# Optimization experiments

Hardware: AMD Instinct MI355X
Metric: run time of the kernel (lower is better)

The kernel has to match this reference:

```python
import jax, jax.numpy as jnp
import numpy as np

B, T, D, H = 2, 2048, 1024, 16
HD = D // H


def setup_inputs() -> dict:
    key = jax.random.key(0)
    ks = jax.random.split(key, 9)
    s = 1.0 / np.sqrt(D)
    return {
        "x": jax.random.normal(ks[0], (B, T, D), dtype=jnp.float32),
        "Wq": jax.random.normal(ks[1], (D, D), dtype=jnp.float32) * s,
        "bq": jnp.zeros((D,), dtype=jnp.float32),
        "Wk": jax.random.normal(ks[2], (D, D), dtype=jnp.float32) * s,
        "bk": jnp.zeros((D,), dtype=jnp.float32),
        "Wv": jax.random.normal(ks[3], (D, D), dtype=jnp.float32) * s,
        "bv": jnp.zeros((D,), dtype=jnp.float32),
        "Wo": jax.random.normal(ks[4], (D, D), dtype=jnp.float32) * s,
        "bo": jnp.zeros((D,), dtype=jnp.float32),
    }


def reference(x, Wq, bq, Wk, bk, Wv, bv, Wo, bo):
    b, t, d = x.shape
    # projections, split heads: (b, h, t, hd)
    def heads(y):
        return y.reshape(b, t, H, HD).transpose(0, 2, 1, 3)
    Q = heads(x @ Wq + bq)
    K = heads(x @ Wk + bk)
    V = heads(x @ Wv + bv)
    # scores scaled by sqrt(d) (full embed dim, faithful to source)
    score = jnp.einsum("bhid,bhjd->bhij", Q, K) / jnp.sqrt(jnp.float32(d))
    causal = jnp.triu(jnp.ones((t, t), dtype=bool), k=1)  # (t, t)
    score = jnp.where(causal, jnp.float32(-1e10), score)
    # FAITHFUL quirk: softmax over the HEAD axis (torch dim=1 of [b,h,t,t])
    weight = jax.nn.softmax(score, axis=1)
    out = jnp.einsum("bhij,bhjd->bhid", weight, V)
    out = out.transpose(0, 2, 1, 3).reshape(b, t, d)
    return out @ Wo + bo
```

## Files before the change

kernel.cpp:

```cpp
#include <hip/hip_runtime.h>
#include <hip/hip_bf16.h>

#define B_ 2
#define T_ 2048
#define D_ 1024
#define H_ 16

typedef __attribute__((ext_vector_type(8))) short bf16x8;
typedef __attribute__((ext_vector_type(4))) float f32x4;

__device__ __forceinline__ unsigned pack_bf16(float x, float y) {
  unsigned xb = __float_as_uint(x), yb = __float_as_uint(y);
  xb += 0x7fffu + ((xb >> 16) & 1u);
  yb += 0x7fffu + ((yb >> 16) & 1u);
  return (xb >> 16) | (yb & 0xffff0000u);
}
__device__ __forceinline__ unsigned short f2b(float x) {
  unsigned u = __float_as_uint(x);
  u += 0x7fffu + ((u >> 16) & 1u);
  return (unsigned short)(u >> 16);
}
__device__ __forceinline__ float blo(unsigned u) { return __uint_as_float(u << 16); }
__device__ __forceinline__ float bhi(unsigned u) { return __uint_as_float(u & 0xffff0000u); }

__device__ __forceinline__ void gld_lds16(const unsigned short* g, unsigned short* l) {
  __builtin_amdgcn_global_load_lds(
      (const __attribute__((address_space(1))) unsigned int*)g,
      (__attribute__((address_space(3))) unsigned int*)l, 16, 0, 0);
}

__global__ __launch_bounds__(256) void wtrans(const float* __restrict__ W0, const float* __restrict__ W1,
                                              const float* __restrict__ W2, const float* __restrict__ W3,
                                              unsigned short* __restrict__ T0, unsigned short* __restrict__ T1,
                                              unsigned short* __restrict__ T2, unsigned short* __restrict__ T3) {
  const int z = blockIdx.z;
  const float* W = z == 0 ? W0 : z == 1 ? W1 : z == 2 ? W2 : W3;
  unsigned short* T = z == 0 ? T0 : z == 1 ? T1 : z == 2 ? T2 : T3;
  __shared__ unsigned short t[64][72];
  const int k0 = blockIdx.x << 6, n0 = blockIdx.y << 6;
  const int r = threadIdx.x >> 2, c16 = (threadIdx.x & 3) << 4;
#pragma unroll
  for (int e = 0; e < 4; ++e) {
    const float4 v = *(const float4*)&W[(size_t)(k0 + r) * 1024 + n0 + c16 + e * 4];
    t[r][c16 + e * 4 + 0] = f2b(v.x);
    t[r][c16 + e * 4 + 1] = f2b(v.y);
    t[r][c16 + e * 4 + 2] = f2b(v.z);
    t[r][c16 + e * 4 + 3] = f2b(v.w);
  }
  __syncthreads();
  unsigned short o[16];
#pragma unroll
  for (int e = 0; e < 16; ++e) o[e] = t[c16 + e][r];
  unsigned short* dst = &T[(size_t)(n0 + r) * 1024 + k0 + c16];
  *(uint4*)&dst[0] = *(uint4*)&o[0];
  *(uint4*)&dst[8] = *(uint4*)&o[8];
}

__global__ __launch_bounds__(256) void xconv(const float* __restrict__ x, unsigned short* __restrict__ xb) {
  const int i = (blockIdx.x * 256 + threadIdx.x) * 8;
  const float4 a = *(const float4*)&x[i];
  const float4 b = *(const float4*)&x[i + 4];
  uint4 o;
  o.x = pack_bf16(a.x, a.y);
  o.y = pack_bf16(a.z, a.w);
  o.z = pack_bf16(b.x, b.y);
  o.w = pack_bf16(b.z, b.w);
  *(uint4*)&xb[i] = o;
}

template <bool BF16OUT>
__global__ __launch_bounds__(256) void gemm_mfma(const unsigned short* __restrict__ A,
                                                 const unsigned short* __restrict__ B0,
                                                 const unsigned short* __restrict__ B1,
                                                 const unsigned short* __restrict__ B2,
                                                 const float* __restrict__ bi0, const float* __restrict__ bi1,
                                                 const float* __restrict__ bi2,
                                                 void* __restrict__ Y0, void* __restrict__ Y1,
                                                 void* __restrict__ Y2) {
  const int z = blockIdx.z;
  const unsigned short* Bt = z == 0 ? B0 : z == 1 ? B1 : B2;
  const float* bias = z == 0 ? bi0 : z == 1 ? bi1 : bi2;
  void* Y = z == 0 ? Y0 : z == 1 ? Y1 : Y2;
  __shared__ unsigned short As[8192];
  __shared__ unsigned short Bs[8192];
  const int tid = threadIdx.x;
  const int m0 = blockIdx.y << 7, n0 = blockIdx.x << 7;
  const int w = tid >> 6, l = tid & 63, g = l >> 4, c = l & 15;
  const int wm = (w >> 1) << 6, wn = (w & 1) << 6;
  const int srow = tid >> 3;
  const int skel = ((tid & 7) ^ (srow & 7)) << 3;
  const unsigned short* ga = &A[(size_t)(m0 + srow) * 1024 + skel];
  const unsigned short* gb = &Bt[(size_t)(n0 + srow) * 1024 + skel];
  unsigned short* la = &As[tid << 3];
  unsigned short* lb = &Bs[tid << 3];
  f32x4 acc[4][4];
#pragma unroll
  for (int i = 0; i < 4; ++i)
#pragma unroll
    for (int j = 0; j < 4; ++j) acc[i][j] = {0.f, 0.f, 0.f, 0.f};
  for (int k0 = 0; k0 < 1024; k0 += 64) {
    __syncthreads();
#pragma unroll
    for (int a = 0; a < 4; ++a) {
      gld_lds16(ga + (size_t)(a << 5) * 1024 + k0, la + (a << 11));
      gld_lds16(gb + (size_t)(a << 5) * 1024 + k0, lb + (a << 11));
    }
    __syncthreads();
#pragma unroll
    for (int kc = 0; kc < 2; ++kc) {
      bf16x8 af[4], bfr[4];
#pragma unroll
      for (int mf = 0; mf < 4; ++mf) {
        const int m = wm + (mf << 4) + c;
        af[mf] = *(const bf16x8*)&As[((m << 6) + (kc << 5) + (g << 3)) ^ ((m & 7) << 3)];
      }
#pragma unroll
      for (int nf = 0; nf < 4; ++nf) {
        const int n = wn + (nf << 4) + c;
        bfr[nf] = *(const bf16x8*)&Bs[((n << 6) + (kc << 5) + (g << 3)) ^ ((n & 7) << 3)];
      }
#pragma unroll
      for (int mf = 0; mf < 4; ++mf)
#pragma unroll
        for (int nf = 0; nf < 4; ++nf)
          acc[mf][nf] = __builtin_amdgcn_mfma_f32_16x16x32_bf16(af[mf], bfr[nf], acc[mf][nf], 0, 0, 0);
    }
  }
#pragma unroll
  for (int nf = 0; nf < 4; ++nf) {
    const int n = n0 + wn + (nf << 4) + c;
    const float bb = bias[n];
#pragma unroll
    for (int mf = 0; mf < 4; ++mf) {
      const int mrow = m0 + wm + (mf << 4) + (g << 2);
#pragma unroll
      for (int r = 0; r < 4; ++r) {
        const float val = acc[mf][nf][r] + bb;
        if (BF16OUT)
          ((unsigned short*)Y)[((size_t)(mrow + r) << 10) + n] = f2b(val);
        else
          ((float*)Y)[((size_t)(mrow + r) << 10) + n] = val;
      }
    }
  }
}

__global__ __launch_bounds__(256) void transpose_bf16(const unsigned short* __restrict__ Vb,
                                                      unsigned short* __restrict__ Vt) {
  __shared__ unsigned short tile[64][73];
  const int b = blockIdx.z;
  const int t0 = blockIdx.x << 6, d0 = blockIdx.y << 6;
  const int row = threadIdx.x >> 2, cq = (threadIdx.x & 3) << 4;
  const unsigned short* src = &Vb[((size_t)((b << 11) + t0 + row) << 10) + d0 + cq];
  const uint4 va = *(const uint4*)&src[0];
  const uint4 vb2 = *(const uint4*)&src[8];
  const unsigned in[8] = {va.x, va.y, va.z, va.w, vb2.x, vb2.y, vb2.z, vb2.w};
#pragma unroll
  for (int e = 0; e < 8; ++e) {
    tile[row][cq + 2 * e] = (unsigned short)in[e];
    tile[row][cq + 2 * e + 1] = (unsigned short)(in[e] >> 16);
  }
  __syncthreads();
  unsigned o[8];
#pragma unroll
  for (int e = 0; e < 8; ++e)
    o[e] = (unsigned)tile[cq + 2 * e][row] | ((unsigned)tile[cq + 2 * e + 1][row] << 16);
  unsigned short* dst = &Vt[((size_t)((b << 10) + d0 + row) << 11) + t0 + cq];
  uint4 lo, hi;
  lo.x = o[0]; lo.y = o[1]; lo.z = o[2]; lo.w = o[3];
  hi.x = o[4]; hi.y = o[5]; hi.z = o[6]; hi.w = o[7];
  *(uint4*)&dst[0] = lo;
  *(uint4*)&dst[8] = hi;
}

__global__ __launch_bounds__(256) void vblk32(const unsigned short* __restrict__ Vb,
                                              float* __restrict__ Blk) {
  const int b = blockIdx.x >> 6, t = blockIdx.x & 63;
  const int d4 = threadIdx.x << 2;
  float s0 = 0.f, s1 = 0.f, s2 = 0.f, s3 = 0.f;
  for (int j = 0; j < 32; ++j) {
    const uint2 v = *(const uint2*)&Vb[((size_t)((b << 11) + (t << 5) + j) << 10) + d4];
    s0 += blo(v.x); s1 += bhi(v.x); s2 += blo(v.y); s3 += bhi(v.y);
  }
  float4 o = {s0, s1, s2, s3};
  *(float4*)&Blk[((size_t)((b << 6) + t) << 10) + d4] = o;
}

__global__ __launch_bounds__(256) void vsuffix32(const float* __restrict__ Blk, float* __restrict__ Suf) {
  const int idx = blockIdx.x * 256 + threadIdx.x;
  const int b = idx >> 10, d = idx & 1023;
  float s = 0.f;
  Suf[((size_t)(b * 65 + 64) << 10) + d] = 0.f;
  for (int t = 63; t >= 0; --t) {
    s += Blk[((size_t)((b << 6) + t) << 10) + d];
    Suf[((size_t)(b * 65 + t) << 10) + d] = s;
  }
}

__global__ __launch_bounds__(1024, 4) void attn_v15(const unsigned short* __restrict__ Qb,
                                                    const unsigned short* __restrict__ Kb,
                                                    const unsigned short* __restrict__ Vt,
                                                    unsigned short* __restrict__ P0,
                                                    unsigned short* __restrict__ P1,
                                                    unsigned short* __restrict__ P2,
                                                    unsigned short* __restrict__ P3) {
  __shared__ unsigned short Ks[32 * 1024];
  __shared__ unsigned short Vs[1024 * 32];
  __shared__ uint2 Sx[2][8][2][64];

  const int combo = blockIdx.x;
  const int b = combo & 1, s = combo >> 1;
  const int qy = 63 - blockIdx.y;
  const int tid = threadIdx.x;
  const int w = tid >> 6, l = tid & 63, g = l >> 4, c = l & 15;
  const int isub = w >> 3, hp = w & 7;
  const float SC = 0.04508422f;
  unsigned short* AOp = s == 0 ? P0 : s == 1 ? P1 : s == 2 ? P2 : P3;

#pragma unroll
  for (int ph = 0; ph < 2; ++ph) {
    const int q = ph ? (63 - qy) : qy;
    const int nt = q + 1;
    const int i0w = (q << 5) + (isub << 4);
    const int ib = i0w + c;

    const unsigned short* qbase =
        &Qb[((size_t)((b << 11) + i0w + c) << 10) + (hp << 7) + (g << 3)];
    bf16x8 qf[4];
    qf[0] = *(const bf16x8*)&qbase[0];
    qf[1] = *(const bf16x8*)&qbase[32];
    qf[2] = *(const bf16x8*)&qbase[64];
    qf[3] = *(const bf16x8*)&qbase[96];

    f32x4 acc[2][4];
#pragma unroll
    for (int hh = 0; hh < 2; ++hh)
#pragma unroll
      for (int cc = 0; cc < 4; ++cc) acc[hh][cc] = {0.f, 0.f, 0.f, 0.f};

#pragma unroll
    for (int e = 0; e < 2; ++e) {
      const int eh = e ? (7 - s) : s;
      const int lo = eh << 3;
      const int hi = (lo + 8) < nt ? (lo + 8) : nt;
      for (int ts = lo; ts < hi; ++ts) {
        const int j0 = ts << 5;
        __syncthreads();
#pragma unroll
        for (int kk = 0; kk < 4; ++kk) {
          const int qq = tid + (kk << 10);
          const int row = qq >> 7, cc8 = qq & 127;
          const int scc = cc8 ^ (row & 7);
          gld_lds16(&Kb[((size_t)((b << 11) + j0 + row) << 10) + (scc << 3)], &Ks[qq << 3]);
        }
#pragma unroll
        for (int kk = 0; kk < 4; ++kk) {
          const int qq = tid + (kk << 10);
          const int d = qq >> 2, jc = qq & 3;
          const int jcg = jc ^ ((d >> 1) & 3);
          gld_lds16(&Vt[(((size_t)((b << 10) + d)) << 11) + j0 + (jcg << 3)], &Vs[qq << 3]);
        }
        __syncthreads();

        f32x4 ex0[2], ex1[2];
        f32x4 ps0 = {0.f, 0.f, 0.f, 0.f}, ps1 = {0.f, 0.f, 0.f, 0.f};
        const int kx = c & 7;
#pragma unroll
        for (int jt = 0; jt < 2; ++jt) {
          const int krow = (jt << 4) + c;
#pragma unroll
          for (int hh = 0; hh < 2; ++hh) {
            const int e8 = ((hp << 1) + hh) << 3;
            const bf16x8 k0 = *(const bf16x8*)&Ks[((krow << 7) + ((e8 + g) ^ kx)) << 3];
            const bf16x8 k1 = *(const bf16x8*)&Ks[((krow << 7) + ((e8 + 4 + g) ^ kx)) << 3];
            f32x4 a = {0.f, 0.f, 0.f, 0.f};
            a = __builtin_amdgcn_mfma_f32_16x16x32_bf16(k0, qf[2 * hh], a, 0, 0, 0);
            a = __builtin_amdgcn_mfma_f32_16x16x32_bf16(k1, qf[2 * hh + 1], a, 0, 0, 0);
            f32x4 ex;
#pragma unroll
            for (int r = 0; r < 4; ++r) ex[r] = exp2f(a[r] * SC);
            if (jt == 0) { ex0[hh] = ex; ps0 += ex; }
            else { ex1[hh] = ex; ps1 += ex; }
          }
        }
        uint2 p0, p1;
        p0.x = pack_bf16(ps0[0], ps0[1]); p0.y = pack_bf16(ps0[2], ps0[3]);
        p1.x = pack_bf16(ps1[0], ps1[1]); p1.y = pack_bf16(ps1[2], ps1[3]);
        Sx[isub][hp][0][l] = p0;
        Sx[isub][hp][1][l] = p1;
        __syncthreads();
        f32x4 s0 = {0.f, 0.f, 0.f, 0.f}, s1 = {0.f, 0.f, 0.f, 0.f};
#pragma unroll
        for (int d8 = 0; d8 < 8; ++d8) {
          const uint2 u0 = Sx[isub][d8][0][l];
          const uint2 u1 = Sx[isub][d8][1][l];
          s0[0] += blo(u0.x); s0[1] += bhi(u0.x); s0[2] += blo(u0.y); s0[3] += bhi(u0.y);
          s1[0] += blo(u1.x); s1[1] += bhi(u1.x); s1[2] += blo(u1.y); s1[3] += bhi(u1.y);
        }
        f32x4 inv0, inv1;
#pragma unroll
        for (int r = 0; r < 4; ++r) {
          inv0[r] = __builtin_amdgcn_rcpf(s0[r]);
          inv1[r] = __builtin_amdgcn_rcpf(s1[r]);
        }
        const int jb = j0 + (g << 2);
#pragma unroll
        for (int hh = 0; hh < 2; ++hh) {
          float w0[4], w1[4];
#pragma unroll
          for (int r = 0; r < 4; ++r) {
            w0[r] = (jb + r > ib) ? 0.0625f : ex0[hh][r] * inv0[r];
            w1[r] = (jb + 16 + r > ib) ? 0.0625f : ex1[hh][r] * inv1[r];
          }
          union { bf16x8 v; unsigned u[4]; } pa;
          pa.u[0] = pack_bf16(w0[0], w0[1]);
          pa.u[1] = pack_bf16(w0[2], w0[3]);
          pa.u[2] = pack_bf16(w1[0], w1[1]);
          pa.u[3] = pack_bf16(w1[2], w1[3]);
#pragma unroll
          for (int cc = 0; cc < 4; ++cc) {
            const int d = (((hp << 1) + hh) << 6) + (cc << 4) + c;
            const int sv = (d >> 1) & 3;
            const int sub = (g & 1) << 2;
            const uint2 lo8 = *(const uint2*)&Vs[((((d << 2) + ((g >> 1) ^ sv)) << 3)) + sub];
            const uint2 hi8 = *(const uint2*)&Vs[((((d << 2) + ((2 + (g >> 1)) ^ sv)) << 3)) + sub];
            union { bf16x8 v; unsigned u[4]; } vf;
            vf.u[0] = lo8.x; vf.u[1] = lo8.y;
            vf.u[2] = hi8.x; vf.u[3] = hi8.y;
            acc[hh][cc] = __builtin_amdgcn_mfma_f32_16x16x32_bf16(pa.v, vf.v, acc[hh][cc], 0, 0, 0);
          }
        }
      }
    }
#pragma unroll
    for (int hh = 0; hh < 2; ++hh)
#pragma unroll
      for (int cc = 0; cc < 4; ++cc) {
        const int d = (((hp << 1) + hh) << 6) + (cc << 4) + c;
#pragma unroll
        for (int r = 0; r < 4; ++r)
          AOp[((size_t)((b << 11) + i0w + (g << 2) + r) << 10) + d] = f2b(acc[hh][cc][r]);
      }
    __syncthreads();
  }
}

__global__ __launch_bounds__(256) void aocvt(const unsigned short* __restrict__ P0,
                                             const unsigned short* __restrict__ P1,
                                             const unsigned short* __restrict__ P2,
                                             const unsigned short* __restrict__ P3,
                                             const float* __restrict__ Suf,
                                             unsigned short* __restrict__ AOb) {
  const int i = (blockIdx.x * 256 + threadIdx.x) << 3;
  const int m = i >> 10;
  const int b = m >> 11;
  const int sufidx = ((m & 2047) >> 5) + 1;
  const int d0 = i & 1023;
  const float* sp = &Suf[((size_t)(b * 65 + sufidx) << 10) + d0];
  const uint4 v0 = *(const uint4*)&P0[i];
  const uint4 v1 = *(const uint4*)&P1[i];
  const uint4 v2 = *(const uint4*)&P2[i];
  const uint4 v3 = *(const uint4*)&P3[i];
  const float4 s0 = *(const float4*)&sp[0];
  const float4 s1 = *(const float4*)&sp[4];
  uint4 o;
  o.x = pack_bf16(blo(v0.x) + blo(v1.x) + blo(v2.x) + blo(v3.x) + 0.0625f * s0.x,
                  bhi(v0.x) + bhi(v1.x) + bhi(v2.x) + bhi(v3.x) + 0.0625f * s0.y);
  o.y = pack_bf16(blo(v0.y) + blo(v1.y) + blo(v2.y) + blo(v3.y) + 0.0625f * s0.z,
                  bhi(v0.y) + bhi(v1.y) + bhi(v2.y) + bhi(v3.y) + 0.0625f * s0.w);
  o.z = pack_bf16(blo(v0.z) + blo(v1.z) + blo(v2.z) + blo(v3.z) + 0.0625f * s1.x,
                  bhi(v0.z) + bhi(v1.z) + bhi(v2.z) + bhi(v3.z) + 0.0625f * s1.y);
  o.w = pack_bf16(blo(v0.w) + blo(v1.w) + blo(v2.w) + blo(v3.w) + 0.0625f * s1.z,
                  bhi(v0.w) + bhi(v1.w) + bhi(v2.w) + bhi(v3.w) + 0.0625f * s1.w);
  *(uint4*)&AOb[i] = o;
}

extern "C" void kernel_launch(void* const* d_in, const int* in_sizes, int n_in,
                              void* d_out, int out_size, void* d_ws, size_t ws_size,
                              hipStream_t stream) {
  (void)in_sizes; (void)n_in; (void)out_size; (void)ws_size;
  const float* x = (const float*)d_in[0];
  const float* Wq = (const float*)d_in[1];
  const float* bq = (const float*)d_in[2];
  const float* Wk = (const float*)d_in[3];
  const float* bk = (const float*)d_in[4];
  const float* Wv = (const float*)d_in[5];
  const float* bv = (const float*)d_in[6];
  const float* Wo = (const float*)d_in[7];
  const float* bo = (const float*)d_in[8];
  float* out = (float*)d_out;
  char* ws = (char*)d_ws;

  const size_t MB = 1024 * 1024;
  unsigned short* xb  = (unsigned short*)(ws);
  unsigned short* Qb  = (unsigned short*)(ws + 8 * MB);
  unsigned short* Kb  = (unsigned short*)(ws + 16 * MB);
  unsigned short* Vb  = (unsigned short*)(ws + 24 * MB);
  unsigned short* Vt  = (unsigned short*)(ws + 32 * MB);
  unsigned short* Wqt = (unsigned short*)(ws + 40 * MB);
  unsigned short* Wkt = (unsigned short*)(ws + 42 * MB);
  unsigned short* Wvt = (unsigned short*)(ws + 44 * MB);
  unsigned short* Wot = (unsigned short*)(ws + 46 * MB);
  unsigned short* AOP2 = (unsigned short*)(ws + 48 * MB);
  unsigned short* AOP3 = (unsigned short*)(ws + 56 * MB);
  float* Blk = (float*)(ws + 40 * MB);
  float* Suf = (float*)(ws + 40 * MB + 512 * 1024);
  unsigned short* AOP0 = xb;
  unsigned short* AOP1 = Vb;
  unsigned short* AOb = Qb;

  hipLaunchKernelGGL(wtrans, dim3(16, 16, 4), dim3(256), 0, stream,
                     Wq, Wk, Wv, Wo, Wqt, Wkt, Wvt, Wot);
  hipLaunchKernelGGL(xconv, dim3(2048), dim3(256), 0, stream, x, xb);
  hipLaunchKernelGGL((gemm_mfma<true>), dim3(8, 32, 3), dim3(256), 0, stream,
                     xb, Wqt, Wkt, Wvt, bq, bk, bv, (void*)Qb, (void*)Kb, (void*)Vb);
  hipLaunchKernelGGL(transpose_bf16, dim3(32, 16, 2), dim3(256), 0, stream, Vb, Vt);
  hipLaunchKernelGGL(vblk32, dim3(128), dim3(256), 0, stream, Vb, Blk);
  hipLaunchKernelGGL(vsuffix32, dim3(8), dim3(256), 0, stream, Blk, Suf);
  hipLaunchKernelGGL(attn_v15, dim3(8, 32), dim3(1024), 0, stream,
                     Qb, Kb, Vt, AOP0, AOP1, AOP2, AOP3);
  hipLaunchKernelGGL(aocvt, dim3(2048), dim3(256), 0, stream,
                     AOP0, AOP1, AOP2, AOP3, Suf, AOb);
  hipLaunchKernelGGL((gemm_mfma<false>), dim3(8, 32, 1), dim3(256), 0, stream,
                     AOb, Wot, Wot, Wot, bo, bo, bo, (void*)out, (void*)out, (void*)out);
}
```

Measured before the change: 211.7 us.

## Double-buffer K/V tiles in attention with 16-row key steps

Attention now walks keys in 16-wide steps instead of 32 and double-buffers the K and V shared-memory tiles, so the next tile's global-to-LDS load is issued while the current tile is being computed. The head-sum exchange buffer now holds full fp32 partial sums rather than bf16-packed pairs. The PV product switches to the 16x16x16 MFMA, and the causal mask check is skipped for tiles that are fully below the diagonal. This hides load latency and trims conversion work, at the cost of twice as many loop iterations and the per-iteration barriers that come with them.

```diff
diff --git a/kernel.cpp b/kernel.cpp
--- a/kernel.cpp
+++ b/kernel.cpp
@@ -7,6 +7,7 @@
 #define H_ 16
 
 typedef __attribute__((ext_vector_type(8))) short bf16x8;
+typedef __attribute__((ext_vector_type(4))) short bf16x4;
 typedef __attribute__((ext_vector_type(4))) float f32x4;
 
 __device__ __forceinline__ unsigned pack_bf16(float x, float y) {
@@ -197,16 +198,16 @@
   }
 }
 
-__global__ __launch_bounds__(1024, 4) void attn_v15(const unsigned short* __restrict__ Qb,
+__global__ __launch_bounds__(1024, 4) void attn_v16(const unsigned short* __restrict__ Qb,
                                                     const unsigned short* __restrict__ Kb,
                                                     const unsigned short* __restrict__ Vt,
                                                     unsigned short* __restrict__ P0,
                                                     unsigned short* __restrict__ P1,
                                                     unsigned short* __restrict__ P2,
                                                     unsigned short* __restrict__ P3) {
-  __shared__ unsigned short Ks[32 * 1024];
-  __shared__ unsigned short Vs[1024 * 32];
-  __shared__ uint2 Sx[2][8][2][64];
+  __shared__ unsigned short Ks[2][16 * 1024];
+  __shared__ unsigned short Vs[2][1024 * 16];
+  __shared__ f32x4 Sx[2][8][64];
 
   const int combo = blockIdx.x;
   const int b = combo & 1, s = combo >> 1;
@@ -217,10 +218,15 @@
   const float SC = 0.04508422f;
   unsigned short* AOp = s == 0 ? P0 : s == 1 ? P1 : s == 2 ? P2 : P3;
 
+  const int krow0 = tid >> 7, kc8 = tid & 127;
+  const int kscc = kc8 ^ (krow0 & 7);
+  const int krow1 = (tid + 1024) >> 7, kc8b = tid & 127;
+  const int ksccb = kc8b ^ (krow1 & 7);
+
 #pragma unroll
   for (int ph = 0; ph < 2; ++ph) {
     const int q = ph ? (63 - qy) : qy;
-    const int nt = q + 1;
+    const int nt16 = (q + 1) << 1;
     const int i0w = (q << 5) + (isub << 4);
     const int ib = i0w + c;
 
@@ -241,95 +247,96 @@
 #pragma unroll
     for (int e = 0; e < 2; ++e) {
       const int eh = e ? (7 - s) : s;
-      const int lo = eh << 3;
-      const int hi = (lo + 8) < nt ? (lo + 8) : nt;
+      const int lo = eh << 4;
+      const int hi = (lo + 16) < nt16 ? (lo + 16) : nt16;
+      if (lo >= hi) continue;
+
+      {
+        const int j0e = lo << 4;
+        gld_lds16(&Kb[((size_t)((b << 11) + j0e + krow0) << 10) + (kscc << 3)], &Ks[0][tid << 3]);
+        gld_lds16(&Kb[((size_t)((b << 11) + j0e + krow1) << 10) + (ksccb << 3)],
+                  &Ks[0][(tid + 1024) << 3]);
+#pragma unroll
+        for (int kk = 0; kk < 2; ++kk) {
+          const int qq = tid + (kk << 10);
+          const int d = qq >> 1, jc = qq & 1;
+          const int joff = ((jc << 1) ^ (((d >> 2) & 1) << 1)) << 2;
+          gld_lds16(&Vt[(((size_t)((b << 10) + d)) << 11) + j0e + joff], &Vs[0][qq << 3]);
+        }
+      }
+      __syncthreads();
+
       for (int ts = lo; ts < hi; ++ts) {
-        const int j0 = ts << 5;
+        const int cur = (ts - lo) & 1;
+        if (ts + 1 < hi) {
+          const int j0e = (ts + 1) << 4;
+          gld_lds16(&Kb[((size_t)((b << 11) + j0e + krow0) << 10) + (kscc << 3)],
+                    &Ks[cur ^ 1][tid << 3]);
+          gld_lds16(&Kb[((size_t)((b << 11) + j0e + krow1) << 10) + (ksccb << 3)],
+                    &Ks[cur ^ 1][(tid + 1024) << 3]);
+#pragma unroll
+          for (int kk = 0; kk < 2; ++kk) {
+            const int qq = tid + (kk << 10);
+            const int d = qq >> 1, jc = qq & 1;
+            const int joff = ((jc << 1) ^ (((d >> 2) & 1) << 1)) << 2;
+            gld_lds16(&Vt[(((size_t)((b << 10) + d)) << 11) + j0e + joff],
+                      &Vs[cur ^ 1][qq << 3]);
+          }
+        }
+        const int j0 = ts << 4;
+        const int kx = c & 7;
+        f32x4 ex[2];
+        f32x4 ps = {0.f, 0.f, 0.f, 0.f};
+#pragma unroll
+        for (int hh = 0; hh < 2; ++hh) {
+          const int hc = ((hp << 1) + hh) << 3;
+          const bf16x8 k0 = *(const bf16x8*)&Ks[cur][((c << 7) + ((hc + g) ^ kx)) << 3];
+          const bf16x8 k1 = *(const bf16x8*)&Ks[cur][((c << 7) + ((hc + 4 + g) ^ kx)) << 3];
+          f32x4 a = {0.f, 0.f, 0.f, 0.f};
+          a = __builtin_amdgcn_mfma_f32_16x16x32_bf16(k0, qf[2 * hh], a, 0, 0, 0);
+          a = __builtin_amdgcn_mfma_f32_16x16x32_bf16(k1, qf[2 * hh + 1], a, 0, 0, 0);
+#pragma unroll
+          for (int r = 0; r < 4; ++r) ex[hh][r] = exp2f(a[r] * SC);
+          ps += ex[hh];
+        }
+        Sx[isub][hp][l] = ps;
         __syncthreads();
-#pragma unroll
-        for (int kk = 0; kk < 4; ++kk) {
-          const int qq = tid + (kk << 10);
-          const int row = qq >> 7, cc8 = qq & 127;
-          const int scc = cc8 ^ (row & 7);
-          gld_lds16(&Kb[((size_t)((b << 11) + j0 + row) << 10) + (scc << 3)], &Ks[qq << 3]);
+        f32x4 sum = Sx[isub][0][l];
+#pragma unroll
+        for (int d8 = 1; d8 < 8; ++d8) sum += Sx[isub][d8][l];
+        f32x4 inv;
+#pragma unroll
+        for (int r = 0; r < 4; ++r) inv[r] = __builtin_amdgcn_rcpf(sum[r]);
+        float wv[2][4];
+        if (j0 + 15 <= i0w) {
+#pragma unroll
+          for (int hh = 0; hh < 2; ++hh)
+#pragma unroll
+            for (int r = 0; r < 4; ++r) wv[hh][r] = ex[hh][r] * inv[r];
+        } else {
+          const int jb = j0 + (g << 2);
+#pragma unroll
+          for (int hh = 0; hh < 2; ++hh)
+#pragma unroll
+            for (int r = 0; r < 4; ++r)
+              wv[hh][r] = (jb + r > ib) ? 0.0625f : ex[hh][r] * inv[r];
         }
 #pragma unroll
-        for (int kk = 0; kk < 4; ++kk) {
-          const int qq = tid + (kk << 10);
-          const int d = qq >> 2, jc = qq & 3;
-          const int jcg = jc ^ ((d >> 1) & 3);
-          gld_lds16(&Vt[(((size_t)((b << 10) + d)) << 11) + j0 + (jcg << 3)], &Vs[qq << 3]);
+        for (int hh = 0; hh < 2; ++hh) {
+          union { bf16x4 v; unsigned u[2]; } pa;
+          pa.u[0] = pack_bf16(wv[hh][0], wv[hh][1]);
+          pa.u[1] = pack_bf16(wv[hh][2], wv[hh][3]);
+#pragma unroll
+          for (int cc = 0; cc < 4; ++cc) {
+            const int d = (((hp << 1) + hh) << 6) + (cc << 4) + c;
+            const int up = g ^ (((d >> 2) & 1) << 1);
+            union { bf16x4 v; unsigned u[2]; } vf;
+            *(uint2*)&vf = *(const uint2*)&Vs[cur][(d << 4) + (up << 2)];
+            acc[hh][cc] =
+                __builtin_amdgcn_mfma_f32_16x16x16bf16_1k(pa.v, vf.v, acc[hh][cc], 0, 0, 0);
+          }
         }
         __syncthreads();
-
-        f32x4 ex0[2], ex1[2];
-        f32x4 ps0 = {0.f, 0.f, 0.f, 0.f}, ps1 = {0.f, 0.f, 0.f, 0.f};
-        const int kx = c & 7;
-#pragma unroll
-        for (int jt = 0; jt < 2; ++jt) {
-          const int krow = (jt << 4) + c;
-#pragma unroll
-          for (int hh = 0; hh < 2; ++hh) {
-            const int e8 = ((hp << 1) + hh) << 3;
-            const bf16x8 k0 = *(const bf16x8*)&Ks[((krow << 7) + ((e8 + g) ^ kx)) << 3];
-            const bf16x8 k1 = *(const bf16x8*)&Ks[((krow << 7) + ((e8 + 4 + g) ^ kx)) << 3];
-            f32x4 a = {0.f, 0.f, 0.f, 0.f};
-            a = __builtin_amdgcn_mfma_f32_16x16x32_bf16(k0, qf[2 * hh], a, 0, 0, 0);
-            a = __builtin_amdgcn_mfma_f32_16x16x32_bf16(k1, qf[2 * hh + 1], a, 0, 0, 0);
-            f32x4 ex;
-#pragma unroll
-            for (int r = 0; r < 4; ++r) ex[r] = exp2f(a[r] * SC);
-            if (jt == 0) { ex0[hh] = ex; ps0 += ex; }
-            else { ex1[hh] = ex; ps1 += ex; }
-          }
-        }
-        uint2 p0, p1;
-        p0.x = pack_bf16(ps0[0], ps0[1]); p0.y = pack_bf16(ps0[2], ps0[3]);
-        p1.x = pack_bf16(ps1[0], ps1[1]); p1.y = pack_bf16(ps1[2], ps1[3]);
-        Sx[isub][hp][0][l] = p0;
-        Sx[isub][hp][1][l] = p1;
-        __syncthreads();
-        f32x4 s0 = {0.f, 0.f, 0.f, 0.f}, s1 = {0.f, 0.f, 0.f, 0.f};
-#pragma unroll
-        for (int d8 = 0; d8 < 8; ++d8) {
-          const uint2 u0 = Sx[isub][d8][0][l];
-          const uint2 u1 = Sx[isub][d8][1][l];
-          s0[0] += blo(u0.x); s0[1] += bhi(u0.x); s0[2] += blo(u0.y); s0[3] += bhi(u0.y);
-          s1[0] += blo(u1.x); s1[1] += bhi(u1.x); s1[2] += blo(u1.y); s1[3] += bhi(u1.y);
-        }
-        f32x4 inv0, inv1;
-#pragma unroll
-        for (int r = 0; r < 4; ++r) {
-          inv0[r] = __builtin_amdgcn_rcpf(s0[r]);
-          inv1[r] = __builtin_amdgcn_rcpf(s1[r]);
-        }
-        const int jb = j0 + (g << 2);
-#pragma unroll
-        for (int hh = 0; hh < 2; ++hh) {
-          float w0[4], w1[4];
-#pragma unroll
-          for (int r = 0; r < 4; ++r) {
-            w0[r] = (jb + r > ib) ? 0.0625f : ex0[hh][r] * inv0[r];
-            w1[r] = (jb + 16 + r > ib) ? 0.0625f : ex1[hh][r] * inv1[r];
-          }
-          union { bf16x8 v; unsigned u[4]; } pa;
-          pa.u[0] = pack_bf16(w0[0], w0[1]);
-          pa.u[1] = pack_bf16(w0[2], w0[3]);
-          pa.u[2] = pack_bf16(w1[0], w1[1]);
-          pa.u[3] = pack_bf16(w1[2], w1[3]);
-#pragma unroll
-          for (int cc = 0; cc < 4; ++cc) {
-            const int d = (((hp << 1) + hh) << 6) + (cc << 4) + c;
-            const int sv = (d >> 1) & 3;
-            const int sub = (g & 1) << 2;
-            const uint2 lo8 = *(const uint2*)&Vs[((((d << 2) + ((g >> 1) ^ sv)) << 3)) + sub];
-            const uint2 hi8 = *(const uint2*)&Vs[((((d << 2) + ((2 + (g >> 1)) ^ sv)) << 3)) + sub];
-            union { bf16x8 v; unsigned u[4]; } vf;
-            vf.u[0] = lo8.x; vf.u[1] = lo8.y;
-            vf.u[2] = hi8.x; vf.u[3] = hi8.y;
-            acc[hh][cc] = __builtin_amdgcn_mfma_f32_16x16x32_bf16(pa.v, vf.v, acc[hh][cc], 0, 0, 0);
-          }
-        }
       }
     }
 #pragma unroll
@@ -341,7 +348,6 @@
         for (int r = 0; r < 4; ++r)
           AOp[((size_t)((b << 11) + i0w + (g << 2) + r) << 10) + d] = f2b(acc[hh][cc][r]);
       }
-    __syncthreads();
   }
 }
 
@@ -417,7 +423,7 @@
   hipLaunchKernelGGL(transpose_bf16, dim3(32, 16, 2), dim3(256), 0, stream, Vb, Vt);
   hipLaunchKernelGGL(vblk32, dim3(128), dim3(256), 0, stream, Vb, Blk);
   hipLaunchKernelGGL(vsuffix32, dim3(8), dim3(256), 0, stream, Blk, Suf);
-  hipLaunchKernelGGL(attn_v15, dim3(8, 32), dim3(1024), 0, stream,
+  hipLaunchKernelGGL(attn_v16, dim3(8, 32), dim3(1024), 0, stream,
                      Qb, Kb, Vt, AOP0, AOP1, AOP2, AOP3);
   hipLaunchKernelGGL(aocvt, dim3(2048), dim3(256), 0, stream,
                      AOP0, AOP1, AOP2, AOP3, Suf, AOb);
```

After: 194.0 us. 8.4% less time.
